# Kernel optimization log

Measured on AMD Instinct MI355X. Metric: run time of the kernel, lower is better.

The kernel has to match this reference:

```python
import jax, jax.numpy as jnp
import numpy as np

B, L, D = 4, 2048, 512
DK = D // 2
DH = 256.0  # scaling denominator


def _skew(QE):
    # QE: [B, L, M] with M == L (relative position logits via skewing trick)
    b, l, m = QE.shape
    pad = jnp.zeros((b, l, 1), QE.dtype)
    cat = jnp.concatenate([pad, QE], axis=2)      # [B, L, M+1]
    reshaped = cat.reshape(b, m + 1, l)           # [B, M+1, L]
    return reshaped[:, 1:, :]                     # [B, M, L]


def setup_inputs() -> dict:
    key = jax.random.key(0)
    ks = jax.random.split(key, 7)
    return {
        "inputQ": jax.random.normal(ks[0], (B, L, D), jnp.float32),
        "inputK": jax.random.normal(ks[1], (B, L, D), jnp.float32),
        "inputV": jax.random.normal(ks[2], (B, L, D), jnp.float32),
        "Wq": jax.random.normal(ks[3], (D, DK), jnp.float32) * 0.02,
        "Wk": jax.random.normal(ks[4], (D, DK), jnp.float32) * 0.02,
        "Wv": jax.random.normal(ks[5], (D, D), jnp.float32) * 0.02,
        "E": jax.random.normal(ks[6], (L, DK), jnp.float32) * 0.02,
    }


def reference(inputQ, inputK, inputV, Wq, Wk, Wv, E):
    Q = jnp.einsum('bld,dk->blk', inputQ, Wq)   # [B, L, DK]
    K = jnp.einsum('bld,dk->blk', inputK, Wk)   # [B, L, DK]
    V = jnp.einsum('bld,de->ble', inputV, Wv)   # [B, L, D]
    QE = jnp.einsum('blk,mk->blm', Q, E)        # [B, L, max_seq]
    Srel = _skew(QE)                             # [B, L, L]
    QKt = jnp.einsum('blk,bmk->blm', Q, K)      # [B, L, L]
    attn = jax.nn.softmax((QKt + Srel) / jnp.sqrt(jnp.float32(DH)), axis=-1)
    return jnp.einsum('blm,bme->ble', attn, V)  # [B, L, D]
```

## Files before the change

### kernel.cpp

```cpp
#include <hip/hip_runtime.h>
#include <hip/hip_bf16.h>

#define BB 4
#define LL 2048
#define DD 512
#define DKK 256

typedef __bf16 bf16;
typedef __bf16 bf16x4 __attribute__((ext_vector_type(4)));
typedef __bf16 bf16x8 __attribute__((ext_vector_type(8)));
typedef float f32x4 __attribute__((ext_vector_type(4)));

__device__ __forceinline__ void async_ld16(const bf16* g, bf16* l) {
    __builtin_amdgcn_global_load_lds(
        (const __attribute__((address_space(1))) void*)g,
        (__attribute__((address_space(3))) void*)l, 16, 0, 0);
}

__global__ void conv3_f32_bf16(const float* __restrict__ a, const float* __restrict__ bq,
                               const float* __restrict__ c,
                               bf16* __restrict__ oa, bf16* __restrict__ ob,
                               bf16* __restrict__ oc, int n4) {
    const float* in = (blockIdx.y == 0) ? a : (blockIdx.y == 1) ? bq : c;
    bf16* out = (blockIdx.y == 0) ? oa : (blockIdx.y == 1) ? ob : oc;
    int i = blockIdx.x * 256 + threadIdx.x;
    if (i < n4) {
        f32x4 v = *(const f32x4*)(in + (size_t)i * 4);
        bf16x4 o;
        #pragma unroll
        for (int j = 0; j < 4; ++j) o[j] = (bf16)v[j];
        *(bf16x4*)(out + (size_t)i * 4) = o;
    }
}

__global__ void prep_misc(const float* __restrict__ E, const float* __restrict__ Wq,
                          const float* __restrict__ Wk, const float* __restrict__ Wv,
                          bf16* __restrict__ Eb, bf16* __restrict__ WqT,
                          bf16* __restrict__ WkT, bf16* __restrict__ WvT) {
    int y = blockIdx.y;
    int idx = blockIdx.x * 256 + threadIdx.x;
    if (y == 0) {
        if (idx < (LL * DKK) / 4) {
            f32x4 v = *(const f32x4*)(E + (size_t)idx * 4);
            bf16x4 o;
            #pragma unroll
            for (int j = 0; j < 4; ++j) o[j] = (bf16)v[j];
            *(bf16x4*)(Eb + (size_t)idx * 4) = o;
        }
    } else if (y == 1) {
        if (idx < DD * DKK) { int r = idx / DKK, c = idx % DKK; WqT[(size_t)c * DD + r] = (bf16)Wq[idx]; }
    } else if (y == 2) {
        if (idx < DD * DKK) { int r = idx / DKK, c = idx % DKK; WkT[(size_t)c * DD + r] = (bf16)Wk[idx]; }
    } else {
        if (idx < DD * DD)  { int r = idx / DD,  c = idx % DD;  WvT[(size_t)c * DD + r] = (bf16)Wv[idx]; }
    }
}

__launch_bounds__(256, 2)
__global__ void gemm_qkv(const bf16* __restrict__ Xq, const bf16* __restrict__ WqT,
                         bf16* __restrict__ Qw,
                         const bf16* __restrict__ Xk, const bf16* __restrict__ WkT,
                         bf16* __restrict__ Kw,
                         const bf16* __restrict__ Xv, const bf16* __restrict__ WvT,
                         bf16* __restrict__ Vt)
{
    __shared__ bf16 Als[128 * 32];
    __shared__ bf16 Bls[128 * 32];
    __shared__ bf16 tbuf[64 * 136];

    int tid  = threadIdx.x;
    int lane = tid & 63;
    int wid  = tid >> 6;
    int l15  = lane & 15;
    int quad = lane >> 4;

    int bid  = blockIdx.x;
    int mode = (bid < 128) ? 0 : (bid < 256) ? 1 : 2;
    int idx  = bid - ((mode == 0) ? 0 : (mode == 1) ? 128 : 256);
    int nb   = (mode == 2) ? 4 : 2;
    int gx = idx % nb;
    int gy = idx / nb;
    int N  = (mode == 2) ? DD : DKK;
    const bf16* A  = (mode == 0) ? Xq  : (mode == 1) ? Xk  : Xv;
    const bf16* Bw = (mode == 0) ? WqT : (mode == 1) ? WkT : WvT;
    const int K = DD;

    const bf16* Ab = A + (size_t)gy * 128 * K;
    const bf16* Bb = Bw + (size_t)gx * 128 * K;

    int rl = lane >> 2;
    int sl = lane & 3;
    int half = wid & 1;
    const bf16* gsrc = (wid < 2) ? Ab : Bb;
    bf16* ldst = (wid < 2) ? Als : Bls;

    const bf16* gptr[4];
    #pragma unroll
    for (int u = 0; u < 4; ++u) {
        int inst = half * 4 + u;
        int row  = inst * 16 + rl;
        int c    = (sl - (row >> 1)) & 3;
        gptr[u] = gsrc + (size_t)row * K + c * 8;
    }

    f32x4 acc[4][4];
    #pragma unroll
    for (int i = 0; i < 4; ++i)
        #pragma unroll
        for (int j = 0; j < 4; ++j) acc[i][j] = 0;

    for (int k0 = 0; k0 < K; k0 += 32) {
        #pragma unroll
        for (int u = 0; u < 4; ++u) {
            async_ld16(gptr[u], ldst + (half * 4 + u) * 512);
            gptr[u] += 32;
        }
        __syncthreads();
        bf16x8 fA[4], fB[4];
        #pragma unroll
        for (int rt = 0; rt < 4; ++rt) {
            int row = (wid & 1) * 64 + rt * 16 + l15;
            int s   = (quad + (row >> 1)) & 3;
            fA[rt] = *(const bf16x8*)&Als[row * 32 + s * 8];
        }
        #pragma unroll
        for (int ct = 0; ct < 4; ++ct) {
            int col = (wid >> 1) * 64 + ct * 16 + l15;
            int s   = (quad + (col >> 1)) & 3;
            fB[ct] = *(const bf16x8*)&Bls[col * 32 + s * 8];
        }
        #pragma unroll
        for (int rt = 0; rt < 4; ++rt)
            #pragma unroll
            for (int ct = 0; ct < 4; ++ct)
                acc[rt][ct] = __builtin_amdgcn_mfma_f32_16x16x32_bf16(
                                  fA[rt], fB[ct], acc[rt][ct], 0, 0, 0);
        __syncthreads();
    }

    if (mode == 2) {
        #pragma unroll
        for (int p = 0; p < 2; ++p) {
            if ((wid >> 1) == p) {
                #pragma unroll
                for (int rt = 0; rt < 4; ++rt)
                    #pragma unroll
                    for (int ct = 0; ct < 4; ++ct)
                        #pragma unroll
                        for (int r = 0; r < 4; ++r)
                            tbuf[(ct * 16 + l15) * 136
                                 + (wid & 1) * 64 + rt * 16 + quad * 4 + r]
                                = (bf16)acc[rt][ct][r];
            }
            __syncthreads();
            int row = tid >> 2, c0 = (tid & 3) * 32;
            bf16* dst = Vt + (size_t)(gx * 128 + p * 64 + row) * (BB * LL)
                           + (size_t)gy * 128 + c0;
            #pragma unroll
            for (int q = 0; q < 4; ++q)
                *(bf16x8*)(dst + q * 8) = *(const bf16x8*)&tbuf[row * 136 + c0 + q * 8];
            __syncthreads();
        }
    } else {
        bf16* Cb = (mode == 0) ? Qw : Kw;
        int m0 = gy * 128 + (wid & 1) * 64;
        int n0 = gx * 128 + (wid >> 1) * 64;
        #pragma unroll
        for (int rt = 0; rt < 4; ++rt)
            #pragma unroll
            for (int ct = 0; ct < 4; ++ct)
                #pragma unroll
                for (int r = 0; r < 4; ++r) {
                    int m = m0 + rt * 16 + quad * 4 + r;
                    int n = n0 + ct * 16 + l15;
                    Cb[(size_t)m * N + n] = (bf16)acc[rt][ct][r];
                }
    }
}

__launch_bounds__(256, 2)
__global__ void gemm_srel(const bf16* __restrict__ A, const bf16* __restrict__ B,
                          bf16* __restrict__ C, long aStride, long cStride)
{
    __shared__ bf16 Als[128 * 32];
    __shared__ bf16 Bls[128 * 32];

    int tid  = threadIdx.x;
    int lane = tid & 63;
    int wid  = tid >> 6;
    int l15  = lane & 15;
    int quad = lane >> 4;
    const int N = LL, K = DKK;
    int nb = N >> 7;
    int gx = blockIdx.x % nb;
    int gy = blockIdx.x / nb;

    const bf16* Ab = A + (size_t)blockIdx.y * aStride + (size_t)gy * 128 * K;
    const bf16* Bb = B + (size_t)gx * 128 * K;

    int rl = lane >> 2;
    int sl = lane & 3;
    int half = wid & 1;
    const bf16* gsrc = (wid < 2) ? Ab : Bb;
    bf16* ldst = (wid < 2) ? Als : Bls;

    const bf16* gptr[4];
    #pragma unroll
    for (int u = 0; u < 4; ++u) {
        int inst = half * 4 + u;
        int row  = inst * 16 + rl;
        int c    = (sl - (row >> 1)) & 3;
        gptr[u] = gsrc + (size_t)row * K + c * 8;
    }

    f32x4 acc[4][4];
    #pragma unroll
    for (int i = 0; i < 4; ++i)
        #pragma unroll
        for (int j = 0; j < 4; ++j) acc[i][j] = 0;

    for (int k0 = 0; k0 < K; k0 += 32) {
        #pragma unroll
        for (int u = 0; u < 4; ++u) {
            async_ld16(gptr[u], ldst + (half * 4 + u) * 512);
            gptr[u] += 32;
        }
        __syncthreads();
        bf16x8 fA[4], fB[4];
        #pragma unroll
        for (int rt = 0; rt < 4; ++rt) {
            int row = (wid & 1) * 64 + rt * 16 + l15;
            int s   = (quad + (row >> 1)) & 3;
            fA[rt] = *(const bf16x8*)&Als[row * 32 + s * 8];
        }
        #pragma unroll
        for (int ct = 0; ct < 4; ++ct) {
            int col = (wid >> 1) * 64 + ct * 16 + l15;
            int s   = (quad + (col >> 1)) & 3;
            fB[ct] = *(const bf16x8*)&Bls[col * 32 + s * 8];
        }
        #pragma unroll
        for (int rt = 0; rt < 4; ++rt)
            #pragma unroll
            for (int ct = 0; ct < 4; ++ct)
                acc[rt][ct] = __builtin_amdgcn_mfma_f32_16x16x32_bf16(
                                  fA[rt], fB[ct], acc[rt][ct], 0, 0, 0);
        __syncthreads();
    }

    bf16* Cb = C + (size_t)blockIdx.y * cStride;
    int m0 = gy * 128 + (wid & 1) * 64;
    int n0 = gx * 128 + (wid >> 1) * 64;
    #pragma unroll
    for (int rt = 0; rt < 4; ++rt)
        #pragma unroll
        for (int ct = 0; ct < 4; ++ct)
            #pragma unroll
            for (int r = 0; r < 4; ++r) {
                int row = m0 + rt * 16 + quad * 4 + r;
                int c   = n0 + ct * 16 + l15;
                bool lower = (c >= LL - 1 - row);
                int dr = lower ? row : row - 1;
                int dc = lower ? c - (LL - 1 - row) : c + row + 1;
                if (lower || row >= 1)
                    Cb[(size_t)dr * LL + dc] = (bf16)acc[rt][ct][r];
            }
}

__launch_bounds__(256, 2)
__global__ void attn_kernel(const bf16* __restrict__ Qw, const bf16* __restrict__ Kw,
                            const bf16* __restrict__ Vt, const bf16* __restrict__ Srel,
                            float* __restrict__ out)
{
    __shared__ bf16  Klds[64 * 256];
    __shared__ bf16  Vlds[256 * 64];
    __shared__ bf16  SrelL[32 * 72];
    __shared__ bf16  Ps[32][72];
    __shared__ float pmax[32][4];
    __shared__ float aSt[32];

    int tid  = threadIdx.x;
    int lane = tid & 63;
    int wid  = tid >> 6;
    int l15  = lane & 15;
    int quad = lane >> 4;

    int xcd = blockIdx.x & 7;
    int b   = xcd >> 1;
    int dh  = xcd & 1;
    int i0  = (blockIdx.x >> 3) * 32;

    const bf16* Qb = Qw + (size_t)b * LL * DKK;
    const bf16* Kb = Kw + (size_t)b * LL * DKK;
    const bf16* Sb = Srel + (size_t)b * LL * LL;
    const bf16* Vb = Vt + (size_t)(dh * 256) * (BB * LL) + (size_t)b * LL;

    const bf16* kptr[8];
    const bf16* vptr[8];
    #pragma unroll
    for (int u = 0; u < 8; ++u) {
        int inst = wid * 8 + u;
        int j_ = inst * 2 + (lane >> 5);
        int ck = ((lane & 31) - j_) & 31;
        kptr[u] = Kb + (size_t)j_ * DKK + ck * 8;
        int d_ = inst * 8 + (lane >> 3);
        int cv = ((lane & 7) - d_) & 7;
        vptr[u] = Vb + (size_t)d_ * (BB * LL) + cv * 8;
    }

    bf16x8 Qreg[2][8];
    #pragma unroll
    for (int rt = 0; rt < 2; ++rt)
        #pragma unroll
        for (int ks = 0; ks < 8; ++ks)
            Qreg[rt][ks] = *(const bf16x8*)(Qb + (size_t)(i0 + rt * 16 + l15) * DKK
                                            + ks * 32 + quad * 8);

    f32x4 accO[2][4];
    #pragma unroll
    for (int rt = 0; rt < 2; ++rt)
        #pragma unroll
        for (int nt = 0; nt < 4; ++nt) accO[rt][nt] = 0;

    float mreg0 = -1e30f, mreg1 = -1e30f;
    float lreg0 = 0.f, lreg1 = 0.f;

    asm volatile("s_waitcnt vmcnt(0)" ::: "memory");

    int srow = i0 + (tid >> 3), ssg = tid & 7;
    bf16x8 srelNext = *(const bf16x8*)(Sb + (size_t)srow * LL + ssg * 8);
    const bf16* sPtr = Sb + (size_t)srow * LL + ssg * 8 + 64;
    __builtin_amdgcn_sched_barrier(0);
    #pragma unroll
    for (int u = 0; u < 8; ++u) {
        async_ld16(kptr[u], Klds + (wid * 8 + u) * 512);
        kptr[u] += 64 * DKK;
    }
    __builtin_amdgcn_sched_barrier(0);
    *(bf16x8*)&SrelL[(tid >> 3) * 72 + (tid & 7) * 8] = srelNext;
    asm volatile("s_waitcnt lgkmcnt(0)\ns_barrier" ::: "memory");

    int jrow = wid * 16 + l15;

    for (int j0 = 0; j0 < LL; j0 += 64) {
        bool notlast = (j0 + 64 < LL);

        if (j0 == 0) asm volatile("s_waitcnt vmcnt(0)" ::: "memory");
        else         asm volatile("s_waitcnt vmcnt(8)" ::: "memory");
        bf16x8 kf[8];
        #pragma unroll
        for (int ks = 0; ks < 8; ++ks) {
            int cp = (ks * 4 + quad + jrow) & 31;
            kf[ks] = *(const bf16x8*)&Klds[jrow * 256 + cp * 8];
        }
        asm volatile("s_waitcnt lgkmcnt(0)" ::: "memory");
        __builtin_amdgcn_sched_barrier(0);
        if (notlast) {
            srelNext = *(const bf16x8*)sPtr;
            sPtr += 64;
        }
        __builtin_amdgcn_sched_barrier(0);
        if (notlast) {
            #pragma unroll
            for (int u = 0; u < 8; ++u) {
                async_ld16(kptr[u], Klds + (wid * 8 + u) * 512);
                kptr[u] += 64 * DKK;
            }
        }
        __builtin_amdgcn_sched_barrier(0);

        f32x4 s0 = 0, s1 = 0;
        __builtin_amdgcn_s_setprio(1);
        #pragma unroll
        for (int ks = 0; ks < 8; ++ks) {
            s0 = __builtin_amdgcn_mfma_f32_16x16x32_bf16(kf[ks], Qreg[0][ks], s0, 0, 0, 0);
            s1 = __builtin_amdgcn_mfma_f32_16x16x32_bf16(kf[ks], Qreg[1][ks], s1, 0, 0, 0);
        }
        __builtin_amdgcn_s_setprio(0);

        if (notlast) asm volatile("s_waitcnt vmcnt(9)" ::: "memory");
        else         asm volatile("s_waitcnt vmcnt(0)" ::: "memory");
        if (j0) {
            bf16x8 aF[2][2];
            #pragma unroll
            for (int rt = 0; rt < 2; ++rt)
                #pragma unroll
                for (int kk = 0; kk < 2; ++kk)
                    aF[rt][kk] = *(const bf16x8*)&Ps[rt * 16 + l15][kk * 32 + quad * 8];
            float ar[2][4];
            #pragma unroll
            for (int rt = 0; rt < 2; ++rt)
                #pragma unroll
                for (int r = 0; r < 4; ++r) ar[rt][r] = aSt[rt * 16 + quad * 4 + r];
            bf16x8 vf[4][2];
            #pragma unroll
            for (int nt = 0; nt < 4; ++nt) {
                int dd = wid * 64 + nt * 16 + l15;
                int c0 = (quad + dd) & 7;
                int c1 = (4 + quad + dd) & 7;
                vf[nt][0] = *(const bf16x8*)&Vlds[dd * 64 + c0 * 8];
                vf[nt][1] = *(const bf16x8*)&Vlds[dd * 64 + c1 * 8];
            }
            asm volatile("s_waitcnt lgkmcnt(0)" ::: "memory");
            __builtin_amdgcn_sched_barrier(0);
            #pragma unroll
            for (int u = 0; u < 8; ++u) {
                async_ld16(vptr[u], Vlds + (wid * 8 + u) * 512);
                vptr[u] += 64;
            }
            __builtin_amdgcn_sched_barrier(0);
            __builtin_amdgcn_s_setprio(1);
            #pragma unroll
            for (int nt = 0; nt < 4; ++nt) {
                #pragma unroll
                for (int rt = 0; rt < 2; ++rt) {
                    f32x4 o = accO[rt][nt];
                    o[0] *= ar[rt][0]; o[1] *= ar[rt][1];
                    o[2] *= ar[rt][2]; o[3] *= ar[rt][3];
                    o = __builtin_amdgcn_mfma_f32_16x16x32_bf16(aF[rt][0], vf[nt][0], o, 0, 0, 0);
                    o = __builtin_amdgcn_mfma_f32_16x16x32_bf16(aF[rt][1], vf[nt][1], o, 0, 0, 0);
                    accO[rt][nt] = o;
                }
            }
            __builtin_amdgcn_s_setprio(0);
        } else {
            #pragma unroll
            for (int u = 0; u < 8; ++u) {
                async_ld16(vptr[u], Vlds + (wid * 8 + u) * 512);
                vptr[u] += 64;
            }
        }

        bf16x4 sr0 = *(const bf16x4*)&SrelL[l15 * 72 + wid * 16 + quad * 4];
        bf16x4 sr1 = *(const bf16x4*)&SrelL[(16 + l15) * 72 + wid * 16 + quad * 4];
        int jb = j0 + wid * 16 + quad * 4;
        float v0[4], v1[4];
        #pragma unroll
        for (int r = 0; r < 4; ++r) {
            float a0 = (jb + r == i0 + l15 + 1)      ? 0.f : (float)sr0[r];
            float a1 = (jb + r == i0 + 16 + l15 + 1) ? 0.f : (float)sr1[r];
            v0[r] = (s0[r] + a0) * 0.0625f;
            v1[r] = (s1[r] + a1) * 0.0625f;
        }
        float m0 = fmaxf(fmaxf(v0[0], v0[1]), fmaxf(v0[2], v0[3]));
        float m1 = fmaxf(fmaxf(v1[0], v1[1]), fmaxf(v1[2], v1[3]));
        m0 = fmaxf(m0, __shfl_xor(m0, 16)); m0 = fmaxf(m0, __shfl_xor(m0, 32));
        m1 = fmaxf(m1, __shfl_xor(m1, 16)); m1 = fmaxf(m1, __shfl_xor(m1, 32));
        if (quad == 0) { pmax[l15][wid] = m0; pmax[16 + l15][wid] = m1; }
        asm volatile("s_waitcnt lgkmcnt(0)\ns_barrier" ::: "memory");

        f32x4 pm0 = *(const f32x4*)&pmax[l15][0];
        f32x4 pm1 = *(const f32x4*)&pmax[16 + l15][0];
        float mf0 = fmaxf(fmaxf(fmaxf(pm0[0], pm0[1]), fmaxf(pm0[2], pm0[3])), mreg0);
        float mf1 = fmaxf(fmaxf(fmaxf(pm1[0], pm1[1]), fmaxf(pm1[2], pm1[3])), mreg1);
        float al0 = __expf(mreg0 - mf0); mreg0 = mf0;
        float al1 = __expf(mreg1 - mf1); mreg1 = mf1;
        if (notlast)
            *(bf16x8*)&SrelL[(tid >> 3) * 72 + (tid & 7) * 8] = srelNext;
        float ps0 = 0.f, ps1 = 0.f;
        bf16x4 pv0, pv1;
        #pragma unroll
        for (int r = 0; r < 4; ++r) {
            float e0 = __expf(v0[r] - mf0); ps0 += e0; pv0[r] = (bf16)e0;
            float e1 = __expf(v1[r] - mf1); ps1 += e1; pv1[r] = (bf16)e1;
        }
        ps0 += __shfl_xor(ps0, 16); ps0 += __shfl_xor(ps0, 32);
        ps1 += __shfl_xor(ps1, 16); ps1 += __shfl_xor(ps1, 32);
        lreg0 = al0 * lreg0 + ps0;
        lreg1 = al1 * lreg1 + ps1;
        *(bf16x4*)&Ps[l15][wid * 16 + quad * 4]      = pv0;
        *(bf16x4*)&Ps[16 + l15][wid * 16 + quad * 4] = pv1;
        if (wid == 0 && quad == 0) { aSt[l15] = al0; aSt[16 + l15] = al1; }
        asm volatile("s_waitcnt lgkmcnt(0)\ns_barrier" ::: "memory");
    }

    asm volatile("s_waitcnt vmcnt(0)" ::: "memory");
    {
        bf16x8 aF[2][2];
        #pragma unroll
        for (int rt = 0; rt < 2; ++rt)
            #pragma unroll
            for (int kk = 0; kk < 2; ++kk)
                aF[rt][kk] = *(const bf16x8*)&Ps[rt * 16 + l15][kk * 32 + quad * 8];
        float ar[2][4];
        #pragma unroll
        for (int rt = 0; rt < 2; ++rt)
            #pragma unroll
            for (int r = 0; r < 4; ++r) ar[rt][r] = aSt[rt * 16 + quad * 4 + r];
        bf16x8 vf[4][2];
        #pragma unroll
        for (int nt = 0; nt < 4; ++nt) {
            int dd = wid * 64 + nt * 16 + l15;
            int c0 = (quad + dd) & 7;
            int c1 = (4 + quad + dd) & 7;
            vf[nt][0] = *(const bf16x8*)&Vlds[dd * 64 + c0 * 8];
            vf[nt][1] = *(const bf16x8*)&Vlds[dd * 64 + c1 * 8];
        }
        #pragma unroll
        for (int nt = 0; nt < 4; ++nt) {
            #pragma unroll
            for (int rt = 0; rt < 2; ++rt) {
                f32x4 o = accO[rt][nt];
                o[0] *= ar[rt][0]; o[1] *= ar[rt][1];
                o[2] *= ar[rt][2]; o[3] *= ar[rt][3];
                o = __builtin_amdgcn_mfma_f32_16x16x32_bf16(aF[rt][0], vf[nt][0], o, 0, 0, 0);
                o = __builtin_amdgcn_mfma_f32_16x16x32_bf16(aF[rt][1], vf[nt][1], o, 0, 0, 0);
                accO[rt][nt] = o;
            }
        }
    }

    if (quad == 0) { pmax[l15][wid] = lreg0; pmax[16 + l15][wid] = lreg1; }
    asm volatile("s_waitcnt lgkmcnt(0)\ns_barrier" ::: "memory");
    float lr[2][4];
    #pragma unroll
    for (int rt = 0; rt < 2; ++rt)
        #pragma unroll
        for (int r = 0; r < 4; ++r) {
            f32x4 lp = *(const f32x4*)&pmax[rt * 16 + quad * 4 + r][0];
            lr[rt][r] = 1.f / (lp[0] + lp[1] + lp[2] + lp[3]);
        }
    #pragma unroll
    for (int rt = 0; rt < 2; ++rt)
        #pragma unroll
        for (int nt = 0; nt < 4; ++nt)
            #pragma unroll
            for (int r = 0; r < 4; ++r) {
                int i = i0 + rt * 16 + quad * 4 + r;
                int d = dh * 256 + wid * 64 + nt * 16 + l15;
                out[((size_t)b * LL + i) * DD + d] = accO[rt][nt][r] * lr[rt][r];
            }
}

extern "C" void kernel_launch(void* const* d_in, const int* in_sizes, int n_in,
                              void* d_out, int out_size, void* d_ws, size_t ws_size,
                              hipStream_t stream) {
    const float* inQ = (const float*)d_in[0];
    const float* inK = (const float*)d_in[1];
    const float* inV = (const float*)d_in[2];
    const float* Wq  = (const float*)d_in[3];
    const float* Wk  = (const float*)d_in[4];
    const float* Wv  = (const float*)d_in[5];
    const float* E   = (const float*)d_in[6];
    float* out = (float*)d_out;

    char* ws = (char*)d_ws;
    bf16* Qw   = (bf16*)(ws);
    bf16* Kw   = (bf16*)(ws + ((size_t)4  << 20));
    bf16* Vt   = (bf16*)(ws + ((size_t)8  << 20));
    bf16* SrelW= (bf16*)(ws + ((size_t)16 << 20));
    bf16* Xq   = (bf16*)(ws + ((size_t)16 << 20));
    bf16* Xk   = (bf16*)(ws + ((size_t)24 << 20));
    bf16* Xv   = (bf16*)(ws + ((size_t)32 << 20));
    bf16* WqT  = (bf16*)(ws + ((size_t)48 << 20));
    bf16* WkT  = (bf16*)(ws + ((size_t)48 << 20) + 262144);
    bf16* WvT  = (bf16*)(ws + ((size_t)48 << 20) + 524288);
    bf16* Eb   = (bf16*)(ws + ((size_t)49 << 20));

    conv3_f32_bf16<<<dim3(4096, 3), 256, 0, stream>>>(inQ, inK, inV, Xq, Xk, Xv,
                                                      (BB * LL * DD) / 4);
    prep_misc<<<dim3(1024, 4), 256, 0, stream>>>(E, Wq, Wk, Wv, Eb, WqT, WkT, WvT);

    gemm_qkv<<<512, 256, 0, stream>>>(Xq, WqT, Qw, Xk, WkT, Kw, Xv, WvT, Vt);
    gemm_srel<<<dim3(16 * 16, BB), 256, 0, stream>>>(Qw, Eb, SrelW,
                                                     (long)LL * DKK, (long)LL * LL);
    attn_kernel<<<dim3(BB * 64 * 2), 256, 0, stream>>>(Qw, Kw, Vt, SrelW, out);
}
```

Measured before the change: 229.7 us.

## Split attention block across 8 waves with per-wave query/key halves

Doubles the attention block to 512 threads (8 waves). Each wave now handles one 16-row query half and one 16-key quarter for QK^T, and a 32-column slice of the output for PV, which cuts per-wave registers and work. The V prefetch is reorganized so V for the current tile is loaded together with K and waited on at a barrier, instead of the previous software-pipelined overlap. This trades more waves for latency hiding against extra barrier synchronization and less load/compute overlap.

```diff
diff --git a/kernel.cpp b/kernel.cpp
--- a/kernel.cpp
+++ b/kernel.cpp
@@ -267,7 +267,7 @@
             }
 }
 
-__launch_bounds__(256, 2)
+__launch_bounds__(512, 4)
 __global__ void attn_kernel(const bf16* __restrict__ Qw, const bf16* __restrict__ Kw,
                             const bf16* __restrict__ Vt, const bf16* __restrict__ Srel,
                             float* __restrict__ out)
@@ -284,6 +284,8 @@
     int wid  = tid >> 6;
     int l15  = lane & 15;
     int quad = lane >> 4;
+    int qh   = wid & 1;
+    int jh   = wid >> 1;
 
     int xcd = blockIdx.x & 7;
     int b   = xcd >> 1;
@@ -295,187 +297,118 @@
     const bf16* Sb = Srel + (size_t)b * LL * LL;
     const bf16* Vb = Vt + (size_t)(dh * 256) * (BB * LL) + (size_t)b * LL;
 
-    const bf16* kptr[8];
-    const bf16* vptr[8];
-    #pragma unroll
-    for (int u = 0; u < 8; ++u) {
-        int inst = wid * 8 + u;
-        int j_ = inst * 2 + (lane >> 5);
+    const bf16* kptr[4];
+    const bf16* vptr[4];
+    #pragma unroll
+    for (int u = 0; u < 4; ++u) {
+        int kinst = wid * 4 + u;
+        int j_ = kinst * 2 + (lane >> 5);
         int ck = ((lane & 31) - j_) & 31;
         kptr[u] = Kb + (size_t)j_ * DKK + ck * 8;
-        int d_ = inst * 8 + (lane >> 3);
+        int d_ = kinst * 8 + (lane >> 3);
         int cv = ((lane & 7) - d_) & 7;
         vptr[u] = Vb + (size_t)d_ * (BB * LL) + cv * 8;
     }
 
-    bf16x8 Qreg[2][8];
+    bf16x8 Qreg[8];
+    #pragma unroll
+    for (int ks = 0; ks < 8; ++ks)
+        Qreg[ks] = *(const bf16x8*)(Qb + (size_t)(i0 + qh * 16 + l15) * DKK
+                                    + ks * 32 + quad * 8);
+
+    f32x4 accO[2][2];
     #pragma unroll
     for (int rt = 0; rt < 2; ++rt)
         #pragma unroll
-        for (int ks = 0; ks < 8; ++ks)
-            Qreg[rt][ks] = *(const bf16x8*)(Qb + (size_t)(i0 + rt * 16 + l15) * DKK
-                                            + ks * 32 + quad * 8);
-
-    f32x4 accO[2][4];
-    #pragma unroll
-    for (int rt = 0; rt < 2; ++rt)
-        #pragma unroll
-        for (int nt = 0; nt < 4; ++nt) accO[rt][nt] = 0;
-
-    float mreg0 = -1e30f, mreg1 = -1e30f;
-    float lreg0 = 0.f, lreg1 = 0.f;
-
-    asm volatile("s_waitcnt vmcnt(0)" ::: "memory");
-
-    int srow = i0 + (tid >> 3), ssg = tid & 7;
-    bf16x8 srelNext = *(const bf16x8*)(Sb + (size_t)srow * LL + ssg * 8);
-    const bf16* sPtr = Sb + (size_t)srow * LL + ssg * 8 + 64;
+        for (int nt = 0; nt < 2; ++nt) accO[rt][nt] = 0;
+
+    float mreg = -1e30f;
+    float lreg = 0.f;
+
+    int srowl = tid >> 4;
+    int scol  = (tid & 15) * 4;
+    const bf16* sPtr = Sb + (size_t)(i0 + srowl) * LL + scol;
+    bf16x4 srelNext = *(const bf16x4*)sPtr;
+    sPtr += 64;
     __builtin_amdgcn_sched_barrier(0);
     #pragma unroll
-    for (int u = 0; u < 8; ++u) {
-        async_ld16(kptr[u], Klds + (wid * 8 + u) * 512);
+    for (int u = 0; u < 4; ++u) {
+        async_ld16(kptr[u], Klds + (wid * 4 + u) * 512);
         kptr[u] += 64 * DKK;
+        async_ld16(vptr[u], Vlds + (wid * 4 + u) * 512);
+        vptr[u] += 64;
     }
     __builtin_amdgcn_sched_barrier(0);
-    *(bf16x8*)&SrelL[(tid >> 3) * 72 + (tid & 7) * 8] = srelNext;
-    asm volatile("s_waitcnt lgkmcnt(0)\ns_barrier" ::: "memory");
-
-    int jrow = wid * 16 + l15;
+    *(bf16x4*)&SrelL[srowl * 72 + scol] = srelNext;
+    asm volatile("s_waitcnt vmcnt(0) lgkmcnt(0)\ns_barrier" ::: "memory");
+
+    int jrow = jh * 16 + l15;
 
     for (int j0 = 0; j0 < LL; j0 += 64) {
         bool notlast = (j0 + 64 < LL);
 
-        if (j0 == 0) asm volatile("s_waitcnt vmcnt(0)" ::: "memory");
-        else         asm volatile("s_waitcnt vmcnt(8)" ::: "memory");
         bf16x8 kf[8];
         #pragma unroll
         for (int ks = 0; ks < 8; ++ks) {
             int cp = (ks * 4 + quad + jrow) & 31;
             kf[ks] = *(const bf16x8*)&Klds[jrow * 256 + cp * 8];
         }
-        asm volatile("s_waitcnt lgkmcnt(0)" ::: "memory");
+        if (notlast) {
+            srelNext = *(const bf16x4*)sPtr;
+            sPtr += 64;
+        }
         __builtin_amdgcn_sched_barrier(0);
+        f32x4 s0 = 0;
+        __builtin_amdgcn_s_setprio(1);
+        #pragma unroll
+        for (int ks = 0; ks < 8; ++ks)
+            s0 = __builtin_amdgcn_mfma_f32_16x16x32_bf16(kf[ks], Qreg[ks], s0, 0, 0, 0);
+        __builtin_amdgcn_s_setprio(0);
+
+        bf16x4 sr = *(const bf16x4*)&SrelL[(qh * 16 + l15) * 72 + jh * 16 + quad * 4];
+        int iq = i0 + qh * 16 + l15;
+        int jb = j0 + jh * 16 + quad * 4;
+        float v[4];
+        #pragma unroll
+        for (int r = 0; r < 4; ++r) {
+            float a = (jb + r == iq + 1) ? 0.f : (float)sr[r];
+            v[r] = (s0[r] + a) * 0.0625f;
+        }
+        float m0 = fmaxf(fmaxf(v[0], v[1]), fmaxf(v[2], v[3]));
+        m0 = fmaxf(m0, __shfl_xor(m0, 16));
+        m0 = fmaxf(m0, __shfl_xor(m0, 32));
+        if (quad == 0) pmax[qh * 16 + l15][jh] = m0;
+        asm volatile("s_waitcnt lgkmcnt(0)\ns_barrier" ::: "memory");
+
         if (notlast) {
-            srelNext = *(const bf16x8*)sPtr;
-            sPtr += 64;
-        }
-        __builtin_amdgcn_sched_barrier(0);
-        if (notlast) {
-            #pragma unroll
-            for (int u = 0; u < 8; ++u) {
-                async_ld16(kptr[u], Klds + (wid * 8 + u) * 512);
+            #pragma unroll
+            for (int u = 0; u < 4; ++u) {
+                async_ld16(kptr[u], Klds + (wid * 4 + u) * 512);
                 kptr[u] += 64 * DKK;
             }
         }
         __builtin_amdgcn_sched_barrier(0);
-
-        f32x4 s0 = 0, s1 = 0;
-        __builtin_amdgcn_s_setprio(1);
-        #pragma unroll
-        for (int ks = 0; ks < 8; ++ks) {
-            s0 = __builtin_amdgcn_mfma_f32_16x16x32_bf16(kf[ks], Qreg[0][ks], s0, 0, 0, 0);
-            s1 = __builtin_amdgcn_mfma_f32_16x16x32_bf16(kf[ks], Qreg[1][ks], s1, 0, 0, 0);
-        }
-        __builtin_amdgcn_s_setprio(0);
-
-        if (notlast) asm volatile("s_waitcnt vmcnt(9)" ::: "memory");
-        else         asm volatile("s_waitcnt vmcnt(0)" ::: "memory");
-        if (j0) {
-            bf16x8 aF[2][2];
-            #pragma unroll
-            for (int rt = 0; rt < 2; ++rt)
-                #pragma unroll
-                for (int kk = 0; kk < 2; ++kk)
-                    aF[rt][kk] = *(const bf16x8*)&Ps[rt * 16 + l15][kk * 32 + quad * 8];
-            float ar[2][4];
-            #pragma unroll
-            for (int rt = 0; rt < 2; ++rt)
-                #pragma unroll
-                for (int r = 0; r < 4; ++r) ar[rt][r] = aSt[rt * 16 + quad * 4 + r];
-            bf16x8 vf[4][2];
-            #pragma unroll
-            for (int nt = 0; nt < 4; ++nt) {
-                int dd = wid * 64 + nt * 16 + l15;
-                int c0 = (quad + dd) & 7;
-                int c1 = (4 + quad + dd) & 7;
-                vf[nt][0] = *(const bf16x8*)&Vlds[dd * 64 + c0 * 8];
-                vf[nt][1] = *(const bf16x8*)&Vlds[dd * 64 + c1 * 8];
-            }
-            asm volatile("s_waitcnt lgkmcnt(0)" ::: "memory");
-            __builtin_amdgcn_sched_barrier(0);
-            #pragma unroll
-            for (int u = 0; u < 8; ++u) {
-                async_ld16(vptr[u], Vlds + (wid * 8 + u) * 512);
-                vptr[u] += 64;
-            }
-            __builtin_amdgcn_sched_barrier(0);
-            __builtin_amdgcn_s_setprio(1);
-            #pragma unroll
-            for (int nt = 0; nt < 4; ++nt) {
-                #pragma unroll
-                for (int rt = 0; rt < 2; ++rt) {
-                    f32x4 o = accO[rt][nt];
-                    o[0] *= ar[rt][0]; o[1] *= ar[rt][1];
-                    o[2] *= ar[rt][2]; o[3] *= ar[rt][3];
-                    o = __builtin_amdgcn_mfma_f32_16x16x32_bf16(aF[rt][0], vf[nt][0], o, 0, 0, 0);
-                    o = __builtin_amdgcn_mfma_f32_16x16x32_bf16(aF[rt][1], vf[nt][1], o, 0, 0, 0);
-                    accO[rt][nt] = o;
-                }
-            }
-            __builtin_amdgcn_s_setprio(0);
-        } else {
-            #pragma unroll
-            for (int u = 0; u < 8; ++u) {
-                async_ld16(vptr[u], Vlds + (wid * 8 + u) * 512);
-                vptr[u] += 64;
-            }
-        }
-
-        bf16x4 sr0 = *(const bf16x4*)&SrelL[l15 * 72 + wid * 16 + quad * 4];
-        bf16x4 sr1 = *(const bf16x4*)&SrelL[(16 + l15) * 72 + wid * 16 + quad * 4];
-        int jb = j0 + wid * 16 + quad * 4;
-        float v0[4], v1[4];
+        f32x4 pm = *(const f32x4*)&pmax[qh * 16 + l15][0];
+        float mf = fmaxf(fmaxf(fmaxf(pm[0], pm[1]), fmaxf(pm[2], pm[3])), mreg);
+        float alpha = __expf(mreg - mf);
+        mreg = mf;
+        if (notlast)
+            *(bf16x4*)&SrelL[srowl * 72 + scol] = srelNext;
+        float ps = 0.f;
+        bf16x4 pv;
         #pragma unroll
         for (int r = 0; r < 4; ++r) {
-            float a0 = (jb + r == i0 + l15 + 1)      ? 0.f : (float)sr0[r];
-            float a1 = (jb + r == i0 + 16 + l15 + 1) ? 0.f : (float)sr1[r];
-            v0[r] = (s0[r] + a0) * 0.0625f;
-            v1[r] = (s1[r] + a1) * 0.0625f;
-        }
-        float m0 = fmaxf(fmaxf(v0[0], v0[1]), fmaxf(v0[2], v0[3]));
-        float m1 = fmaxf(fmaxf(v1[0], v1[1]), fmaxf(v1[2], v1[3]));
-        m0 = fmaxf(m0, __shfl_xor(m0, 16)); m0 = fmaxf(m0, __shfl_xor(m0, 32));
-        m1 = fmaxf(m1, __shfl_xor(m1, 16)); m1 = fmaxf(m1, __shfl_xor(m1, 32));
-        if (quad == 0) { pmax[l15][wid] = m0; pmax[16 + l15][wid] = m1; }
-        asm volatile("s_waitcnt lgkmcnt(0)\ns_barrier" ::: "memory");
-
-        f32x4 pm0 = *(const f32x4*)&pmax[l15][0];
-        f32x4 pm1 = *(const f32x4*)&pmax[16 + l15][0];
-        float mf0 = fmaxf(fmaxf(fmaxf(pm0[0], pm0[1]), fmaxf(pm0[2], pm0[3])), mreg0);
-        float mf1 = fmaxf(fmaxf(fmaxf(pm1[0], pm1[1]), fmaxf(pm1[2], pm1[3])), mreg1);
-        float al0 = __expf(mreg0 - mf0); mreg0 = mf0;
-        float al1 = __expf(mreg1 - mf1); mreg1 = mf1;
-        if (notlast)
-            *(bf16x8*)&SrelL[(tid >> 3) * 72 + (tid & 7) * 8] = srelNext;
-        float ps0 = 0.f, ps1 = 0.f;
-        bf16x4 pv0, pv1;
-        #pragma unroll
-        for (int r = 0; r < 4; ++r) {
-            float e0 = __expf(v0[r] - mf0); ps0 += e0; pv0[r] = (bf16)e0;
-            float e1 = __expf(v1[r] - mf1); ps1 += e1; pv1[r] = (bf16)e1;
-        }
-        ps0 += __shfl_xor(ps0, 16); ps0 += __shfl_xor(ps0, 32);
-        ps1 += __shfl_xor(ps1, 16); ps1 += __shfl_xor(ps1, 32);
-        lreg0 = al0 * lreg0 + ps0;
-        lreg1 = al1 * lreg1 + ps1;
-        *(bf16x4*)&Ps[l15][wid * 16 + quad * 4]      = pv0;
-        *(bf16x4*)&Ps[16 + l15][wid * 16 + quad * 4] = pv1;
-        if (wid == 0 && quad == 0) { aSt[l15] = al0; aSt[16 + l15] = al1; }
-        asm volatile("s_waitcnt lgkmcnt(0)\ns_barrier" ::: "memory");
-    }
-
-    asm volatile("s_waitcnt vmcnt(0)" ::: "memory");
-    {
+            float e = __expf(v[r] - mf);
+            ps += e;
+            pv[r] = (bf16)e;
+        }
+        ps += __shfl_xor(ps, 16);
+        ps += __shfl_xor(ps, 32);
+        lreg = alpha * lreg + ps;
+        *(bf16x4*)&Ps[qh * 16 + l15][jh * 16 + quad * 4] = pv;
+        if (wid < 2 && quad == 0) aSt[qh * 16 + l15] = alpha;
+        asm volatile("s_waitcnt vmcnt(0) lgkmcnt(0)\ns_barrier" ::: "memory");
+
         bf16x8 aF[2][2];
         #pragma unroll
         for (int rt = 0; rt < 2; ++rt)
@@ -487,17 +420,28 @@
         for (int rt = 0; rt < 2; ++rt)
             #pragma unroll
             for (int r = 0; r < 4; ++r) ar[rt][r] = aSt[rt * 16 + quad * 4 + r];
-        bf16x8 vf[4][2];
-        #pragma unroll
-        for (int nt = 0; nt < 4; ++nt) {
-            int dd = wid * 64 + nt * 16 + l15;
+        bf16x8 vf[2][2];
+        #pragma unroll
+        for (int nt = 0; nt < 2; ++nt) {
+            int dd = wid * 32 + nt * 16 + l15;
             int c0 = (quad + dd) & 7;
             int c1 = (4 + quad + dd) & 7;
             vf[nt][0] = *(const bf16x8*)&Vlds[dd * 64 + c0 * 8];
             vf[nt][1] = *(const bf16x8*)&Vlds[dd * 64 + c1 * 8];
         }
-        #pragma unroll
-        for (int nt = 0; nt < 4; ++nt) {
+        asm volatile("s_waitcnt lgkmcnt(0)" ::: "memory");
+        __builtin_amdgcn_sched_barrier(0);
+        if (notlast) {
+            #pragma unroll
+            for (int u = 0; u < 4; ++u) {
+                async_ld16(vptr[u], Vlds + (wid * 4 + u) * 512);
+                vptr[u] += 64;
+            }
+        }
+        __builtin_amdgcn_sched_barrier(0);
+        __builtin_amdgcn_s_setprio(1);
+        #pragma unroll
+        for (int nt = 0; nt < 2; ++nt)
             #pragma unroll
             for (int rt = 0; rt < 2; ++rt) {
                 f32x4 o = accO[rt][nt];
@@ -507,10 +451,10 @@
                 o = __builtin_amdgcn_mfma_f32_16x16x32_bf16(aF[rt][1], vf[nt][1], o, 0, 0, 0);
                 accO[rt][nt] = o;
             }
-        }
-    }
-
-    if (quad == 0) { pmax[l15][wid] = lreg0; pmax[16 + l15][wid] = lreg1; }
+        __builtin_amdgcn_s_setprio(0);
+    }
+
+    if (quad == 0) pmax[qh * 16 + l15][jh] = lreg;
     asm volatile("s_waitcnt lgkmcnt(0)\ns_barrier" ::: "memory");
     float lr[2][4];
     #pragma unroll
@@ -523,11 +467,11 @@
     #pragma unroll
     for (int rt = 0; rt < 2; ++rt)
         #pragma unroll
-        for (int nt = 0; nt < 4; ++nt)
+        for (int nt = 0; nt < 2; ++nt)
             #pragma unroll
             for (int r = 0; r < 4; ++r) {
                 int i = i0 + rt * 16 + quad * 4 + r;
-                int d = dh * 256 + wid * 64 + nt * 16 + l15;
+                int d = dh * 256 + wid * 32 + nt * 16 + l15;
                 out[((size_t)b * LL + i) * DD + d] = accO[rt][nt][r] * lr[rt][r];
             }
 }
@@ -564,5 +508,5 @@
     gemm_qkv<<<512, 256, 0, stream>>>(Xq, WqT, Qw, Xk, WkT, Kw, Xv, WvT, Vt);
     gemm_srel<<<dim3(16 * 16, BB), 256, 0, stream>>>(Qw, Eb, SrelW,
                                                      (long)LL * DKK, (long)LL * LL);
-    attn_kernel<<<dim3(BB * 64 * 2), 256, 0, stream>>>(Qw, Kw, Vt, SrelW, out);
-}
+    attn_kernel<<<dim3(BB * 64 * 2), 512, 0, stream>>>(Qw, Kw, Vt, SrelW, out);
+}
```

Result: slower. 247.6 us (+7.8%).

## Restructure attention softmax through shared scores and double GEMM K-step per barrier

Applied to the files above, without the earlier changes.

The QKV and Srel GEMMs now load two 32-wide K slices per iteration into two LDS buffers, which halves the number of barrier pairs per tile. The attention kernel is reorganised so QK scores are written to an fp32 shared tile. Each group of 8 threads then computes the row max, exponentials and running sum with intra-row shuffles and keeps the m/l state in LDS. The PV product now runs in the same iteration rather than lagging one iteration behind, and the V prefetch is issued ahead of the loop. In exchange this adds an extra LDS round trip for the scores and removes the overlap between PV and softmax.

```diff
diff --git a/kernel.cpp b/kernel.cpp
--- a/kernel.cpp
+++ b/kernel.cpp
@@ -64,8 +64,8 @@
                          const bf16* __restrict__ Xv, const bf16* __restrict__ WvT,
                          bf16* __restrict__ Vt)
 {
-    __shared__ bf16 Als[128 * 32];
-    __shared__ bf16 Bls[128 * 32];
+    __shared__ bf16 Als[2][128 * 32];
+    __shared__ bf16 Bls[2][128 * 32];
     __shared__ bf16 tbuf[64 * 136];
 
     int tid  = threadIdx.x;
@@ -92,7 +92,8 @@
     int sl = lane & 3;
     int half = wid & 1;
     const bf16* gsrc = (wid < 2) ? Ab : Bb;
-    bf16* ldst = (wid < 2) ? Als : Bls;
+    bf16* ldst0 = (wid < 2) ? Als[0] : Bls[0];
+    bf16* ldst1 = (wid < 2) ? Als[1] : Bls[1];
 
     const bf16* gptr[4];
     #pragma unroll
@@ -109,32 +110,36 @@
         #pragma unroll
         for (int j = 0; j < 4; ++j) acc[i][j] = 0;
 
-    for (int k0 = 0; k0 < K; k0 += 32) {
+    for (int k0 = 0; k0 < K; k0 += 64) {
         #pragma unroll
         for (int u = 0; u < 4; ++u) {
-            async_ld16(gptr[u], ldst + (half * 4 + u) * 512);
-            gptr[u] += 32;
+            async_ld16(gptr[u],      ldst0 + (half * 4 + u) * 512);
+            async_ld16(gptr[u] + 32, ldst1 + (half * 4 + u) * 512);
+            gptr[u] += 64;
         }
         __syncthreads();
-        bf16x8 fA[4], fB[4];
-        #pragma unroll
-        for (int rt = 0; rt < 4; ++rt) {
-            int row = (wid & 1) * 64 + rt * 16 + l15;
-            int s   = (quad + (row >> 1)) & 3;
-            fA[rt] = *(const bf16x8*)&Als[row * 32 + s * 8];
-        }
-        #pragma unroll
-        for (int ct = 0; ct < 4; ++ct) {
-            int col = (wid >> 1) * 64 + ct * 16 + l15;
-            int s   = (quad + (col >> 1)) & 3;
-            fB[ct] = *(const bf16x8*)&Bls[col * 32 + s * 8];
-        }
-        #pragma unroll
-        for (int rt = 0; rt < 4; ++rt)
-            #pragma unroll
-            for (int ct = 0; ct < 4; ++ct)
-                acc[rt][ct] = __builtin_amdgcn_mfma_f32_16x16x32_bf16(
-                                  fA[rt], fB[ct], acc[rt][ct], 0, 0, 0);
+        #pragma unroll
+        for (int h2 = 0; h2 < 2; ++h2) {
+            bf16x8 fA[4], fB[4];
+            #pragma unroll
+            for (int rt = 0; rt < 4; ++rt) {
+                int row = (wid & 1) * 64 + rt * 16 + l15;
+                int s   = (quad + (row >> 1)) & 3;
+                fA[rt] = *(const bf16x8*)&Als[h2][row * 32 + s * 8];
+            }
+            #pragma unroll
+            for (int ct = 0; ct < 4; ++ct) {
+                int col = (wid >> 1) * 64 + ct * 16 + l15;
+                int s   = (quad + (col >> 1)) & 3;
+                fB[ct] = *(const bf16x8*)&Bls[h2][col * 32 + s * 8];
+            }
+            #pragma unroll
+            for (int rt = 0; rt < 4; ++rt)
+                #pragma unroll
+                for (int ct = 0; ct < 4; ++ct)
+                    acc[rt][ct] = __builtin_amdgcn_mfma_f32_16x16x32_bf16(
+                                      fA[rt], fB[ct], acc[rt][ct], 0, 0, 0);
+        }
         __syncthreads();
     }
 
@@ -182,8 +187,8 @@
 __global__ void gemm_srel(const bf16* __restrict__ A, const bf16* __restrict__ B,
                           bf16* __restrict__ C, long aStride, long cStride)
 {
-    __shared__ bf16 Als[128 * 32];
-    __shared__ bf16 Bls[128 * 32];
+    __shared__ bf16 Als[2][128 * 32];
+    __shared__ bf16 Bls[2][128 * 32];
 
     int tid  = threadIdx.x;
     int lane = tid & 63;
@@ -202,7 +207,8 @@
     int sl = lane & 3;
     int half = wid & 1;
     const bf16* gsrc = (wid < 2) ? Ab : Bb;
-    bf16* ldst = (wid < 2) ? Als : Bls;
+    bf16* ldst0 = (wid < 2) ? Als[0] : Bls[0];
+    bf16* ldst1 = (wid < 2) ? Als[1] : Bls[1];
 
     const bf16* gptr[4];
     #pragma unroll
@@ -219,32 +225,36 @@
         #pragma unroll
         for (int j = 0; j < 4; ++j) acc[i][j] = 0;
 
-    for (int k0 = 0; k0 < K; k0 += 32) {
+    for (int k0 = 0; k0 < K; k0 += 64) {
         #pragma unroll
         for (int u = 0; u < 4; ++u) {
-            async_ld16(gptr[u], ldst + (half * 4 + u) * 512);
-            gptr[u] += 32;
+            async_ld16(gptr[u],      ldst0 + (half * 4 + u) * 512);
+            async_ld16(gptr[u] + 32, ldst1 + (half * 4 + u) * 512);
+            gptr[u] += 64;
         }
         __syncthreads();
-        bf16x8 fA[4], fB[4];
-        #pragma unroll
-        for (int rt = 0; rt < 4; ++rt) {
-            int row = (wid & 1) * 64 + rt * 16 + l15;
-            int s   = (quad + (row >> 1)) & 3;
-            fA[rt] = *(const bf16x8*)&Als[row * 32 + s * 8];
-        }
-        #pragma unroll
-        for (int ct = 0; ct < 4; ++ct) {
-            int col = (wid >> 1) * 64 + ct * 16 + l15;
-            int s   = (quad + (col >> 1)) & 3;
-            fB[ct] = *(const bf16x8*)&Bls[col * 32 + s * 8];
-        }
-        #pragma unroll
-        for (int rt = 0; rt < 4; ++rt)
-            #pragma unroll
-            for (int ct = 0; ct < 4; ++ct)
-                acc[rt][ct] = __builtin_amdgcn_mfma_f32_16x16x32_bf16(
-                                  fA[rt], fB[ct], acc[rt][ct], 0, 0, 0);
+        #pragma unroll
+        for (int h2 = 0; h2 < 2; ++h2) {
+            bf16x8 fA[4], fB[4];
+            #pragma unroll
+            for (int rt = 0; rt < 4; ++rt) {
+                int row = (wid & 1) * 64 + rt * 16 + l15;
+                int s   = (quad + (row >> 1)) & 3;
+                fA[rt] = *(const bf16x8*)&Als[h2][row * 32 + s * 8];
+            }
+            #pragma unroll
+            for (int ct = 0; ct < 4; ++ct) {
+                int col = (wid >> 1) * 64 + ct * 16 + l15;
+                int s   = (quad + (col >> 1)) & 3;
+                fB[ct] = *(const bf16x8*)&Bls[h2][col * 32 + s * 8];
+            }
+            #pragma unroll
+            for (int rt = 0; rt < 4; ++rt)
+                #pragma unroll
+                for (int ct = 0; ct < 4; ++ct)
+                    acc[rt][ct] = __builtin_amdgcn_mfma_f32_16x16x32_bf16(
+                                      fA[rt], fB[ct], acc[rt][ct], 0, 0, 0);
+        }
         __syncthreads();
     }
 
@@ -274,10 +284,9 @@
 {
     __shared__ bf16  Klds[64 * 256];
     __shared__ bf16  Vlds[256 * 64];
-    __shared__ bf16  SrelL[32 * 72];
+    __shared__ float Ss[32][68];
     __shared__ bf16  Ps[32][72];
-    __shared__ float pmax[32][4];
-    __shared__ float aSt[32];
+    __shared__ float mSt[32], lSt[32], aSt[32];
 
     int tid  = threadIdx.x;
     int lane = tid & 63;
@@ -316,37 +325,38 @@
             Qreg[rt][ks] = *(const bf16x8*)(Qb + (size_t)(i0 + rt * 16 + l15) * DKK
                                             + ks * 32 + quad * 8);
 
+    if (tid < 32) { mSt[tid] = -1e30f; lSt[tid] = 0.f; }
+
     f32x4 accO[2][4];
     #pragma unroll
     for (int rt = 0; rt < 2; ++rt)
         #pragma unroll
         for (int nt = 0; nt < 4; ++nt) accO[rt][nt] = 0;
 
-    float mreg0 = -1e30f, mreg1 = -1e30f;
-    float lreg0 = 0.f, lreg1 = 0.f;
-
     asm volatile("s_waitcnt vmcnt(0)" ::: "memory");
 
-    int srow = i0 + (tid >> 3), ssg = tid & 7;
-    bf16x8 srelNext = *(const bf16x8*)(Sb + (size_t)srow * LL + ssg * 8);
-    const bf16* sPtr = Sb + (size_t)srow * LL + ssg * 8 + 64;
-    __builtin_amdgcn_sched_barrier(0);
     #pragma unroll
     for (int u = 0; u < 8; ++u) {
         async_ld16(kptr[u], Klds + (wid * 8 + u) * 512);
         kptr[u] += 64 * DKK;
     }
     __builtin_amdgcn_sched_barrier(0);
-    *(bf16x8*)&SrelL[(tid >> 3) * 72 + (tid & 7) * 8] = srelNext;
-    asm volatile("s_waitcnt lgkmcnt(0)\ns_barrier" ::: "memory");
+    int srow = i0 + (tid >> 3), ssg = tid & 7;
+    bf16x8 srelCur = *(const bf16x8*)(Sb + (size_t)srow * LL + ssg * 8);
+    const bf16* sPtr = Sb + (size_t)srow * LL + ssg * 8 + 64;
+    __builtin_amdgcn_sched_barrier(0);
+    #pragma unroll
+    for (int u = 0; u < 8; ++u) {
+        async_ld16(vptr[u], Vlds + (wid * 8 + u) * 512);
+        vptr[u] += 64;
+    }
 
     int jrow = wid * 16 + l15;
 
     for (int j0 = 0; j0 < LL; j0 += 64) {
         bool notlast = (j0 + 64 < LL);
 
-        if (j0 == 0) asm volatile("s_waitcnt vmcnt(0)" ::: "memory");
-        else         asm volatile("s_waitcnt vmcnt(8)" ::: "memory");
+        asm volatile("s_waitcnt vmcnt(9)" ::: "memory");
         bf16x8 kf[8];
         #pragma unroll
         for (int ks = 0; ks < 8; ++ks) {
@@ -356,11 +366,6 @@
         asm volatile("s_waitcnt lgkmcnt(0)" ::: "memory");
         __builtin_amdgcn_sched_barrier(0);
         if (notlast) {
-            srelNext = *(const bf16x8*)sPtr;
-            sPtr += 64;
-        }
-        __builtin_amdgcn_sched_barrier(0);
-        if (notlast) {
             #pragma unroll
             for (int u = 0; u < 8; ++u) {
                 async_ld16(kptr[u], Klds + (wid * 8 + u) * 512);
@@ -368,114 +373,64 @@
             }
         }
         __builtin_amdgcn_sched_barrier(0);
-
+        bf16x8 srelNext;
+        if (notlast) {
+            srelNext = *(const bf16x8*)sPtr;
+            sPtr += 64;
+        }
+        __builtin_amdgcn_sched_barrier(0);
         f32x4 s0 = 0, s1 = 0;
         __builtin_amdgcn_s_setprio(1);
         #pragma unroll
         for (int ks = 0; ks < 8; ++ks) {
-            s0 = __builtin_amdgcn_mfma_f32_16x16x32_bf16(kf[ks], Qreg[0][ks], s0, 0, 0, 0);
-            s1 = __builtin_amdgcn_mfma_f32_16x16x32_bf16(kf[ks], Qreg[1][ks], s1, 0, 0, 0);
+            s0 = __builtin_amdgcn_mfma_f32_16x16x32_bf16(Qreg[0][ks], kf[ks], s0, 0, 0, 0);
+            s1 = __builtin_amdgcn_mfma_f32_16x16x32_bf16(Qreg[1][ks], kf[ks], s1, 0, 0, 0);
         }
         __builtin_amdgcn_s_setprio(0);
+        #pragma unroll
+        for (int r = 0; r < 4; ++r) {
+            Ss[quad * 4 + r][wid * 16 + l15]      = s0[r];
+            Ss[16 + quad * 4 + r][wid * 16 + l15] = s1[r];
+        }
+        asm volatile("s_waitcnt lgkmcnt(0)\ns_barrier" ::: "memory");
+
+        {
+            int r = tid >> 3, sg = tid & 7;
+            int i = i0 + r;
+            float v[8];
+            #pragma unroll
+            for (int c = 0; c < 8; ++c) {
+                float sr = (j0 + sg * 8 + c == i + 1) ? 0.f : (float)srelCur[c];
+                v[c] = (Ss[r][sg * 8 + c] + sr) * 0.0625f;
+            }
+            float tmax = v[0];
+            #pragma unroll
+            for (int c = 1; c < 8; ++c) tmax = fmaxf(tmax, v[c]);
+            tmax = fmaxf(tmax, __shfl_xor(tmax, 1));
+            tmax = fmaxf(tmax, __shfl_xor(tmax, 2));
+            tmax = fmaxf(tmax, __shfl_xor(tmax, 4));
+            float mOld = mSt[r], lOld = lSt[r];
+            float mNew = fmaxf(mOld, tmax);
+            float alpha = __expf(mOld - mNew);
+            float ps = 0.f;
+            bf16x8 pv;
+            #pragma unroll
+            for (int c = 0; c < 8; ++c) {
+                float p = __expf(v[c] - mNew);
+                ps += p;
+                pv[c] = (bf16)p;
+            }
+            ps += __shfl_xor(ps, 1);
+            ps += __shfl_xor(ps, 2);
+            ps += __shfl_xor(ps, 4);
+            *(bf16x8*)&Ps[r][sg * 8] = pv;
+            if (sg == 0) { mSt[r] = mNew; lSt[r] = alpha * lOld + ps; aSt[r] = alpha; }
+        }
+        srelCur = srelNext;
+        asm volatile("s_waitcnt lgkmcnt(0)\ns_barrier" ::: "memory");
 
         if (notlast) asm volatile("s_waitcnt vmcnt(9)" ::: "memory");
         else         asm volatile("s_waitcnt vmcnt(0)" ::: "memory");
-        if (j0) {
-            bf16x8 aF[2][2];
-            #pragma unroll
-            for (int rt = 0; rt < 2; ++rt)
-                #pragma unroll
-                for (int kk = 0; kk < 2; ++kk)
-                    aF[rt][kk] = *(const bf16x8*)&Ps[rt * 16 + l15][kk * 32 + quad * 8];
-            float ar[2][4];
-            #pragma unroll
-            for (int rt = 0; rt < 2; ++rt)
-                #pragma unroll
-                for (int r = 0; r < 4; ++r) ar[rt][r] = aSt[rt * 16 + quad * 4 + r];
-            bf16x8 vf[4][2];
-            #pragma unroll
-            for (int nt = 0; nt < 4; ++nt) {
-                int dd = wid * 64 + nt * 16 + l15;
-                int c0 = (quad + dd) & 7;
-                int c1 = (4 + quad + dd) & 7;
-                vf[nt][0] = *(const bf16x8*)&Vlds[dd * 64 + c0 * 8];
-                vf[nt][1] = *(const bf16x8*)&Vlds[dd * 64 + c1 * 8];
-            }
-            asm volatile("s_waitcnt lgkmcnt(0)" ::: "memory");
-            __builtin_amdgcn_sched_barrier(0);
-            #pragma unroll
-            for (int u = 0; u < 8; ++u) {
-                async_ld16(vptr[u], Vlds + (wid * 8 + u) * 512);
-                vptr[u] += 64;
-            }
-            __builtin_amdgcn_sched_barrier(0);
-            __builtin_amdgcn_s_setprio(1);
-            #pragma unroll
-            for (int nt = 0; nt < 4; ++nt) {
-                #pragma unroll
-                for (int rt = 0; rt < 2; ++rt) {
-                    f32x4 o = accO[rt][nt];
-                    o[0] *= ar[rt][0]; o[1] *= ar[rt][1];
-                    o[2] *= ar[rt][2]; o[3] *= ar[rt][3];
-                    o = __builtin_amdgcn_mfma_f32_16x16x32_bf16(aF[rt][0], vf[nt][0], o, 0, 0, 0);
-                    o = __builtin_amdgcn_mfma_f32_16x16x32_bf16(aF[rt][1], vf[nt][1], o, 0, 0, 0);
-                    accO[rt][nt] = o;
-                }
-            }
-            __builtin_amdgcn_s_setprio(0);
-        } else {
-            #pragma unroll
-            for (int u = 0; u < 8; ++u) {
-                async_ld16(vptr[u], Vlds + (wid * 8 + u) * 512);
-                vptr[u] += 64;
-            }
-        }
-
-        bf16x4 sr0 = *(const bf16x4*)&SrelL[l15 * 72 + wid * 16 + quad * 4];
-        bf16x4 sr1 = *(const bf16x4*)&SrelL[(16 + l15) * 72 + wid * 16 + quad * 4];
-        int jb = j0 + wid * 16 + quad * 4;
-        float v0[4], v1[4];
-        #pragma unroll
-        for (int r = 0; r < 4; ++r) {
-            float a0 = (jb + r == i0 + l15 + 1)      ? 0.f : (float)sr0[r];
-            float a1 = (jb + r == i0 + 16 + l15 + 1) ? 0.f : (float)sr1[r];
-            v0[r] = (s0[r] + a0) * 0.0625f;
-            v1[r] = (s1[r] + a1) * 0.0625f;
-        }
-        float m0 = fmaxf(fmaxf(v0[0], v0[1]), fmaxf(v0[2], v0[3]));
-        float m1 = fmaxf(fmaxf(v1[0], v1[1]), fmaxf(v1[2], v1[3]));
-        m0 = fmaxf(m0, __shfl_xor(m0, 16)); m0 = fmaxf(m0, __shfl_xor(m0, 32));
-        m1 = fmaxf(m1, __shfl_xor(m1, 16)); m1 = fmaxf(m1, __shfl_xor(m1, 32));
-        if (quad == 0) { pmax[l15][wid] = m0; pmax[16 + l15][wid] = m1; }
-        asm volatile("s_waitcnt lgkmcnt(0)\ns_barrier" ::: "memory");
-
-        f32x4 pm0 = *(const f32x4*)&pmax[l15][0];
-        f32x4 pm1 = *(const f32x4*)&pmax[16 + l15][0];
-        float mf0 = fmaxf(fmaxf(fmaxf(pm0[0], pm0[1]), fmaxf(pm0[2], pm0[3])), mreg0);
-        float mf1 = fmaxf(fmaxf(fmaxf(pm1[0], pm1[1]), fmaxf(pm1[2], pm1[3])), mreg1);
-        float al0 = __expf(mreg0 - mf0); mreg0 = mf0;
-        float al1 = __expf(mreg1 - mf1); mreg1 = mf1;
-        if (notlast)
-            *(bf16x8*)&SrelL[(tid >> 3) * 72 + (tid & 7) * 8] = srelNext;
-        float ps0 = 0.f, ps1 = 0.f;
-        bf16x4 pv0, pv1;
-        #pragma unroll
-        for (int r = 0; r < 4; ++r) {
-            float e0 = __expf(v0[r] - mf0); ps0 += e0; pv0[r] = (bf16)e0;
-            float e1 = __expf(v1[r] - mf1); ps1 += e1; pv1[r] = (bf16)e1;
-        }
-        ps0 += __shfl_xor(ps0, 16); ps0 += __shfl_xor(ps0, 32);
-        ps1 += __shfl_xor(ps1, 16); ps1 += __shfl_xor(ps1, 32);
-        lreg0 = al0 * lreg0 + ps0;
-        lreg1 = al1 * lreg1 + ps1;
-        *(bf16x4*)&Ps[l15][wid * 16 + quad * 4]      = pv0;
-        *(bf16x4*)&Ps[16 + l15][wid * 16 + quad * 4] = pv1;
-        if (wid == 0 && quad == 0) { aSt[l15] = al0; aSt[16 + l15] = al1; }
-        asm volatile("s_waitcnt lgkmcnt(0)\ns_barrier" ::: "memory");
-    }
-
-    asm volatile("s_waitcnt vmcnt(0)" ::: "memory");
-    {
         bf16x8 aF[2][2];
         #pragma unroll
         for (int rt = 0; rt < 2; ++rt)
@@ -496,6 +451,17 @@
             vf[nt][0] = *(const bf16x8*)&Vlds[dd * 64 + c0 * 8];
             vf[nt][1] = *(const bf16x8*)&Vlds[dd * 64 + c1 * 8];
         }
+        asm volatile("s_waitcnt lgkmcnt(0)" ::: "memory");
+        __builtin_amdgcn_sched_barrier(0);
+        if (notlast) {
+            #pragma unroll
+            for (int u = 0; u < 8; ++u) {
+                async_ld16(vptr[u], Vlds + (wid * 8 + u) * 512);
+                vptr[u] += 64;
+            }
+        }
+        __builtin_amdgcn_sched_barrier(0);
+        __builtin_amdgcn_s_setprio(1);
         #pragma unroll
         for (int nt = 0; nt < 4; ++nt) {
             #pragma unroll
@@ -508,18 +474,13 @@
                 accO[rt][nt] = o;
             }
         }
-    }
-
-    if (quad == 0) { pmax[l15][wid] = lreg0; pmax[16 + l15][wid] = lreg1; }
-    asm volatile("s_waitcnt lgkmcnt(0)\ns_barrier" ::: "memory");
+        __builtin_amdgcn_s_setprio(0);
+    }
     float lr[2][4];
     #pragma unroll
     for (int rt = 0; rt < 2; ++rt)
         #pragma unroll
-        for (int r = 0; r < 4; ++r) {
-            f32x4 lp = *(const f32x4*)&pmax[rt * 16 + quad * 4 + r][0];
-            lr[rt][r] = 1.f / (lp[0] + lp[1] + lp[2] + lp[3]);
-        }
+        for (int r = 0; r < 4; ++r) lr[rt][r] = 1.f / lSt[rt * 16 + quad * 4 + r];
     #pragma unroll
     for (int rt = 0; rt < 2; ++rt)
         #pragma unroll
```

Result: faster. 221.7 us (-3.5%).
